# Kernel tuning notes

Hardware: AMD Instinct MI355X
Metric: run time of the kernel (lower is better)

Reference implementation:

```python
import jax, jax.numpy as jnp
import numpy as np

N_HEAD = 16  # head_dim = C // N_HEAD = 128


def setup_inputs() -> dict:
    key = jax.random.key(0)
    k1, k2, k3 = jax.random.split(key, 3)
    B, T, C = 2, 2048, 2048
    x = jax.random.normal(k1, (B, T, C), dtype=jnp.float32)
    # c_attn: Linear(C, 3*C), no bias; stored as (in, out) for x @ W
    w_attn = jax.random.normal(k2, (C, 3 * C), dtype=jnp.float32) * (1.0 / np.sqrt(C))
    # c_proj: Linear(C, C), no bias
    w_proj = jax.random.normal(k3, (C, C), dtype=jnp.float32) * (1.0 / np.sqrt(C))
    return {"x": x, "w_attn": w_attn, "w_proj": w_proj}


def reference(x, w_attn, w_proj):
    B, T, C = x.shape
    H = N_HEAD
    D = C // H  # head dimension
    qkv = x @ w_attn                      # [B, T, 3C]
    q, k, v = jnp.split(qkv, 3, axis=-1)  # each [B, T, C]
    # [B, T, C] -> [B, H, T, D]
    q = q.reshape(B, T, H, D).transpose(0, 2, 1, 3)
    k = k.reshape(B, T, H, D).transpose(0, 2, 1, 3)
    v = v.reshape(B, T, H, D).transpose(0, 2, 1, 3)
    scale = 1.0 / np.sqrt(D).astype(np.float32)
    att = jnp.einsum('bhqd,bhkd->bhqk', q, k) * scale  # [B, H, T, T]
    causal = jnp.tril(jnp.ones((T, T), dtype=bool))
    att = jnp.where(causal[None, None, :, :], att, jnp.float32(-jnp.inf))
    att = jax.nn.softmax(att, axis=-1)
    y = jnp.einsum('bhqk,bhkd->bhqd', att, v)  # [B, H, T, D]
    y = y.transpose(0, 2, 1, 3).reshape(B, T, C)
    # all_reduce is identity with number_of_workers=1; dropout=0 (eval)
    return y @ w_proj
```

## Files before the change

### kernel.cpp

```cpp
#include <hip/hip_runtime.h>
#include <hip/hip_bf16.h>
#include <stdint.h>

#define TLEN 2048
#define CDIM 2048
#define BDIM 2
#define HDIM 16
#define DHEAD 128
#define QROW ((size_t)(2 * CDIM))

typedef __bf16 bf16x8 __attribute__((ext_vector_type(8)));
typedef float f32x4 __attribute__((ext_vector_type(4)));

__device__ __forceinline__ uint16_t f32_to_bf16(float f) {
    uint32_t u = __builtin_bit_cast(uint32_t, f);
    uint32_t r = (u + 0x7FFFu + ((u >> 16) & 1u)) >> 16;
    return (uint16_t)r;
}
__device__ __forceinline__ float bf16_to_f32(uint32_t h) {
    uint32_t u = h << 16;
    return __builtin_bit_cast(float, u);
}

__device__ __forceinline__ void gload_lds16(const uint16_t* g, uint16_t* l) {
    __builtin_amdgcn_global_load_lds(
        (const __attribute__((address_space(1))) uint32_t*)g,
        (__attribute__((address_space(3))) uint32_t*)l, 16, 0, 0);
}

__global__ void cvt_f32_bf16(const float* __restrict__ in, uint16_t* __restrict__ out, int n) {
    int i = (blockIdx.x * blockDim.x + threadIdx.x) * 4;
    if (i + 3 < n) {
        float4 f = *reinterpret_cast<const float4*>(in + i);
        ushort4 o;
        o.x = f32_to_bf16(f.x);
        o.y = f32_to_bf16(f.y);
        o.z = f32_to_bf16(f.z);
        o.w = f32_to_bf16(f.w);
        *reinterpret_cast<ushort4*>(out + i) = o;
    }
}

__global__ __launch_bounds__(256) void transpose_cvt(const float* __restrict__ in,
                                                     uint16_t* __restrict__ out,
                                                     int R, int Cc) {
    __shared__ uint16_t tile[64][65];
    int c0 = blockIdx.x * 64;
    int r0 = blockIdx.y * 64;
    int tc = threadIdx.x & 63;
    int t4 = threadIdx.x >> 6;
    for (int rr = t4; rr < 64; rr += 4) {
        tile[rr][tc] = f32_to_bf16(in[(size_t)(r0 + rr) * Cc + c0 + tc]);
    }
    __syncthreads();
    int wr = threadIdx.x & 63;
    for (int cc = t4; cc < 64; cc += 4) {
        out[(size_t)(c0 + cc) * R + r0 + wr] = tile[wr][cc];
    }
}


#define RD8(P, OFF) (*reinterpret_cast<const bf16x8*>((P) + (OFF)))

#define RDA(DST, P, MB)                                         \
    _Pragma("unroll") for (int mi = 0; mi < 4; mi++) {          \
        DST[mi][0] = RD8(P, rdAo + ((MB) + mi) * 1024 + kblk0); \
        DST[mi][1] = RD8(P, rdAo + ((MB) + mi) * 1024 + kblk1); \
    }

#define RDB4(DST, P)                                        \
    _Pragma("unroll") for (int ni = 0; ni < 4; ni++) {      \
        DST[ni][0] = RD8(P, rdBo + ni * 1024 + kblk0);      \
        DST[ni][1] = RD8(P, rdBo + ni * 1024 + kblk1);      \
    }

#define MFMA32(MB)                                                    \
    _Pragma("unroll") for (int kk = 0; kk < 2; kk++)                  \
    _Pragma("unroll") for (int mi = 0; mi < 4; mi++)                  \
    _Pragma("unroll") for (int ni = 0; ni < 4; ni++)                  \
        acc[(MB) + mi][ni] = __builtin_amdgcn_mfma_f32_16x16x32_bf16( \
            aA[mi][kk], bB[ni][kk], acc[(MB) + mi][ni], 0, 0, 0);

#define TILE(S, T)                                           \
    {                                                        \
        const int k0 = (T) * 64;                             \
        const uint16_t* pA = As + ((S) + wrow) * 8192;       \
        const uint16_t* pB = Bs + ((S) + bsel) * 8192;       \
        RDB4(bB, pB)                                         \
        RDA(aA, pA, 0)                                       \
        asm volatile("s_waitcnt lgkmcnt(8)" ::: "memory");   \
        __builtin_amdgcn_s_barrier();      \
        if ((T) + 2 < nt) {                                  \
            stB((S), 0, k0 + 128);                           \
            stB((S), 1, k0 + 128);                           \
        }                                                    \
        asm volatile("s_waitcnt lgkmcnt(0)" ::: "memory");   \
        __builtin_amdgcn_sched_barrier(0);                   \
        __builtin_amdgcn_s_setprio(1);                       \
        MFMA32(0)                                            \
        __builtin_amdgcn_s_setprio(0);                       \
        RDA(aA, pA, 4)                                       \
        asm volatile("s_waitcnt lgkmcnt(0)" ::: "memory");   \
        __builtin_amdgcn_s_barrier();      \
        if ((T) + 2 < nt) {                                  \
            stA((S), 0, k0 + 128);                           \
            stA((S), 1, k0 + 128);                           \
        }                                                    \
        __builtin_amdgcn_sched_barrier(0);                   \
        __builtin_amdgcn_s_setprio(1);                       \
        MFMA32(4)                                            \
        __builtin_amdgcn_s_setprio(0);                       \
        if ((T) + 2 < nt) {                                  \
            asm volatile("s_waitcnt vmcnt(8)" ::: "memory"); \
        } else if ((T) + 1 < nt) {                           \
            asm volatile("s_waitcnt vmcnt(0)" ::: "memory"); \
        }                                                    \
        __builtin_amdgcn_s_barrier();       \
        __builtin_amdgcn_sched_barrier(0);                   \
    }

template <int MODE>
__global__ __launch_bounds__(512, 2) void gemm_bf16_256(const uint16_t* __restrict__ A,
                                                        const uint16_t* __restrict__ Bt,
                                                        void* __restrict__ Cp,
                                                        uint16_t* __restrict__ vt,
                                                        int M, int N, int K, int xm) {
    __shared__ __align__(16) uint16_t lds[65536];
    uint16_t* const As = lds;
    uint16_t* const Bs = lds + 32768;

    const int tid = threadIdx.x;
    const int wave = tid >> 6;
    const int lane = tid & 63;
    const int l15 = lane & 15;
    const int quad = lane >> 4;
    const int wrow = wave >> 2;
    const int wcol = wave & 3;
    const int bsel = wcol >> 1;

    const int gm = gridDim.y, gn = gridDim.x;
    const int flat = blockIdx.y * gn + blockIdx.x;
    const int xcd = flat & 7;
    const int j = flat >> 3;
    const int xn = 8 / xm;
    const int RM = gm / xm;
    const int RN = gn / xn;
    const int m_blk = (xcd / xn) * RM + (j % RM);
    const int n_blk = (xcd % xn) * RN + (j / RM);
    const int m0 = m_blk * 256;
    const int n0 = n_blk * 256;

    const int srow = wave * 8 + (lane >> 3);
    const int scol = ((lane & 7) ^ (lane >> 3)) * 8;
    const uint16_t* Ag = A + (size_t)(m0 + srow) * K + scol;
    const uint16_t* Bg = Bt + (size_t)(n0 + srow) * K + scol;
    const int ldsoff = wave * 512;

    const int rdAo = l15 * 64;
    const int rdBo = ((wcol & 1) * 64 + l15) * 64;
    const int kblk0 = (quad ^ (l15 & 7)) * 8;
    const int kblk1 = ((4 + quad) ^ (l15 & 7)) * 8;

    const int nt = K >> 6;
    f32x4 acc[8][4] = {};
    bf16x8 aA[4][2], bB[4][2];

    auto stA = [&](int sb, int h, int kk) {
        const uint16_t* s = Ag + (size_t)(h * 128) * K + kk;
        uint16_t* d = As + (sb + h) * 8192 + ldsoff;
        gload_lds16(s, d);
        gload_lds16(s + (size_t)64 * K, d + 4096);
    };
    auto stB = [&](int sb, int h, int kk) {
        const uint16_t* s = Bg + (size_t)(h * 128) * K + kk;
        uint16_t* d = Bs + (sb + h) * 8192 + ldsoff;
        gload_lds16(s, d);
        gload_lds16(s + (size_t)64 * K, d + 4096);
    };

    stB(0, 0, 0);
    stB(0, 1, 0);
    stA(0, 0, 0);
    stA(0, 1, 0);
    stB(2, 0, 64);
    stB(2, 1, 64);
    stA(2, 0, 64);
    stA(2, 1, 64);
    asm volatile("s_waitcnt vmcnt(8)" ::: "memory");
    __builtin_amdgcn_s_barrier();
    __builtin_amdgcn_sched_barrier(0);

    for (int t = 0; t < nt; t += 2) {
        TILE(0, t)
        TILE(2, t + 1)
    }

    const bool vmode = (MODE == 2) && (n0 >= 2 * CDIM);
#pragma unroll
    for (int mi = 0; mi < 8; mi++)
#pragma unroll
        for (int ni = 0; ni < 4; ni++) {
            if (vmode) {
                int col = n0 + wcol * 64 + ni * 16 + l15;
                int vcol = col - 2 * CDIM;
                int hh = vcol >> 7, d = vcol & 127;
                int rowm = m0 + wrow * 128 + mi * 16 + quad * 4;
                int bb = rowm >> 11, tt = rowm & 2047;
                uint32_t lo = (uint32_t)f32_to_bf16(acc[mi][ni][0]) |
                              ((uint32_t)f32_to_bf16(acc[mi][ni][1]) << 16);
                uint32_t hi = (uint32_t)f32_to_bf16(acc[mi][ni][2]) |
                              ((uint32_t)f32_to_bf16(acc[mi][ni][3]) << 16);
                *reinterpret_cast<uint2*>(
                    vt + ((size_t)((bb * HDIM + hh) * DHEAD + d)) * TLEN + tt) =
                    make_uint2(lo, hi);
            } else {
#pragma unroll
                for (int r = 0; r < 4; r++) {
                    int row = m0 + wrow * 128 + mi * 16 + quad * 4 + r;
                    int col = n0 + wcol * 64 + ni * 16 + l15;
                    float v = acc[mi][ni][r];
                    if (MODE == 2)
                        ((uint16_t*)Cp)[(size_t)row * (2 * CDIM) + col] = f32_to_bf16(v);
                    else if (MODE == 1)
                        ((uint16_t*)Cp)[(size_t)row * N + col] = f32_to_bf16(v);
                    else
                        ((float*)Cp)[(size_t)row * N + col] = v;
                }
            }
        }
}

#define ATT_C1 0.12751743f
#define ATT_C2 17.3123405f

__global__ __launch_bounds__(256) void attn_mfma3(const uint16_t* __restrict__ qkv,
                                                  const uint16_t* __restrict__ vtg,
                                                  uint16_t* __restrict__ y) {
    __shared__ __align__(16) uint16_t Ks[64 * 128];
    __shared__ __align__(16) uint16_t Vts[128 * 64];
    __shared__ __align__(16) uint16_t Ps[4][32 * 72];

    const int tid = threadIdx.x;
    const int wave = tid >> 6;
    const int lane = tid & 63;
    const int l15 = lane & 15;
    const int quad = lane >> 4;
    const int h = blockIdx.y;
    const int b = blockIdx.z;
    const int qblk = (int)gridDim.x - 1 - (int)blockIdx.x;
    const int qbase = qblk * 128 + wave * 32;
    const int kmax = qbase + 31;

    const uint16_t* kg = qkv + (size_t)b * TLEN * QROW + CDIM + h * DHEAD;
    const uint16_t* vg = vtg + (size_t)(b * HDIM + h) * DHEAD * TLEN;
    uint16_t* PsW = Ps[wave];

    int koff[4], voff[4];
#pragma unroll
    for (int i = 0; i < 4; i++) {
        int Lb = (wave * 4 + i) * 64 + lane;
        int key = Lb >> 4;
        int ck = (Lb & 15) ^ (key & 15);
        koff[i] = key * (int)QROW + ck * 8;
        int d = Lb >> 3;
        int cv = (Lb & 7) ^ (d & 7);
        voff[i] = d * TLEN + cv * 8;
    }

    bf16x8 qfrag[2][4];
#pragma unroll
    for (int m = 0; m < 2; m++) {
        const uint16_t* qp =
            qkv + (size_t)(b * TLEN + qbase + m * 16 + l15) * QROW + h * DHEAD + quad * 8;
#pragma unroll
        for (int kc = 0; kc < 4; kc++)
            qfrag[m][kc] = *reinterpret_cast<const bf16x8*>(qp + kc * 32);
    }

    f32x4 oacc[2][8] = {};
    float psum[2] = {0.f, 0.f};

    const int diagT = qblk * 2 + (wave >> 1);
    const int ntiles = qblk * 2 + 2;

    for (int t = 0; t < ntiles; t++) {
        const int j0 = t * 64;
        if (t > 0) __syncthreads();
        {
            const uint16_t* kj = kg + (size_t)j0 * QROW;
            const uint16_t* vj = vg + j0;
#pragma unroll
            for (int i = 0; i < 4; i++) {
                gload_lds16(kj + koff[i], Ks + (wave * 4 + i) * 512);
                gload_lds16(vj + voff[i], Vts + (wave * 4 + i) * 512);
            }
        }
        __syncthreads();
        if (t > diagT) continue;

        const bool masked = (t == diagT);
        const int n0max = masked ? ((kmax - j0) >> 4) : 3;

        f32x4 st[4][2];
#pragma unroll
        for (int n0 = 0; n0 < 4; n0++) {
            if (masked && n0 > n0max) continue;
            bf16x8 kf[4];
#pragma unroll
            for (int kc = 0; kc < 4; kc++) {
                int cpr = (kc * 4 + quad) ^ l15;
                kf[kc] = *reinterpret_cast<const bf16x8*>(
                    Ks + (n0 * 16 + l15) * 128 + cpr * 8);
            }
#pragma unroll
            for (int m = 0; m < 2; m++) {
                f32x4 acc = {};
#pragma unroll
                for (int kc = 0; kc < 4; kc++)
                    acc = __builtin_amdgcn_mfma_f32_16x16x32_bf16(
                        kf[kc], qfrag[m][kc], acc, 0, 0, 0);
                st[n0][m] = acc;
            }
        }

#pragma unroll
        for (int n0 = 0; n0 < 4; n0++) {
            if (masked && n0 > n0max) continue;
#pragma unroll
            for (int m = 0; m < 2; m++) {
                uint32_t pk0, pk1;
                float pv[4];
#pragma unroll
                for (int r = 0; r < 4; r++) {
                    float p = exp2f(st[n0][m][r] * ATT_C1 - ATT_C2);
                    if (masked) {
                        int key = j0 + n0 * 16 + quad * 4 + r;
                        int q = qbase + m * 16 + l15;
                        if (key > q) p = 0.f;
                    }
                    uint32_t pb = f32_to_bf16(p);
                    pv[r] = bf16_to_f32(pb);
                    if (r == 0) pk0 = pb;
                    else if (r == 1) pk0 |= pb << 16;
                    else if (r == 2) pk1 = pb;
                    else pk1 |= pb << 16;
                }
                psum[m] += (pv[0] + pv[1]) + (pv[2] + pv[3]);
                *reinterpret_cast<uint2*>(PsW + (m * 16 + l15) * 72 + n0 * 16 + quad * 4) =
                    make_uint2(pk0, pk1);
            }
        }

        const int kcend = masked ? (((kmax - j0) >> 5) + 1) : 2;
#pragma unroll
        for (int kc = 0; kc < 2; kc++) {
            if (kc >= kcend) continue;
            bf16x8 pf[2];
#pragma unroll
            for (int m = 0; m < 2; m++)
                pf[m] = *reinterpret_cast<const bf16x8*>(
                    PsW + (m * 16 + l15) * 72 + kc * 32 + quad * 8);
#pragma unroll
            for (int n0 = 0; n0 < 8; n0++) {
                int cpr = (kc * 4 + quad) ^ (l15 & 7);
                bf16x8 vf = *reinterpret_cast<const bf16x8*>(
                    Vts + (n0 * 16 + l15) * 64 + cpr * 8);
#pragma unroll
                for (int m = 0; m < 2; m++)
                    oacc[m][n0] = __builtin_amdgcn_mfma_f32_16x16x32_bf16(
                        pf[m], vf, oacc[m][n0], 0, 0, 0);
            }
        }
    }

#pragma unroll
    for (int m = 0; m < 2; m++) {
        float s = psum[m];
        s += __shfl_xor(s, 16);
        s += __shfl_xor(s, 32);
        psum[m] = 1.0f / s;
    }
    uint16_t* ybase = y + (size_t)(b * TLEN + qbase) * CDIM + h * DHEAD;
#pragma unroll
    for (int m = 0; m < 2; m++)
#pragma unroll
        for (int r = 0; r < 4; r++) {
            float inv = __shfl(psum[m], quad * 4 + r);
#pragma unroll
            for (int n0 = 0; n0 < 8; n0++)
                ybase[(size_t)(m * 16 + quad * 4 + r) * CDIM + n0 * 16 + l15] =
                    f32_to_bf16(oacc[m][n0][r] * inv);
        }
}

extern "C" void kernel_launch(void* const* d_in, const int* in_sizes, int n_in,
                              void* d_out, int out_size, void* d_ws, size_t ws_size,
                              hipStream_t stream) {
    const float* x = (const float*)d_in[0];
    const float* w_attn = (const float*)d_in[1];
    const float* w_proj = (const float*)d_in[2];
    float* out = (float*)d_out;

    const int M = BDIM * TLEN;
    const int K = CDIM;
    const int N3 = 3 * CDIM;

    char* ws = (char*)d_ws;
    uint16_t* xb = (uint16_t*)(ws);
    uint16_t* waT = (uint16_t*)(ws + 16777216);
    uint16_t* wpT = (uint16_t*)(ws + 41943040);
    uint16_t* qkp = (uint16_t*)(ws + 50331648);
    uint16_t* vtb = (uint16_t*)(ws + 83886080);
    uint16_t* yb = (uint16_t*)(ws + 100663296);

    cvt_f32_bf16<<<(M * K / 4 + 255) / 256, 256, 0, stream>>>(x, xb, M * K);
    transpose_cvt<<<dim3(N3 / 64, K / 64), 256, 0, stream>>>(w_attn, waT, K, N3);
    transpose_cvt<<<dim3(K / 64, K / 64), 256, 0, stream>>>(w_proj, wpT, K, K);
    gemm_bf16_256<2><<<dim3(N3 / 256, M / 256), 512, 0, stream>>>(xb, waT, (void*)qkp, vtb, M, N3, K, 2);
    attn_mfma3<<<dim3(TLEN / 128, HDIM, BDIM), 256, 0, stream>>>(qkp, vtb, yb);
    gemm_bf16_256<0><<<dim3(K / 256, M / 256), 512, 0, stream>>>(yb, wpT, (void*)out, nullptr, M, K, K, 4);
}
```

Before: 428.6 us.

## Prefetch next K/V tile into registers during attention compute

The attention loop now issues global loads for the next K and V tile into registers before computing on the current tile, then stores them to LDS after a barrier. Previously the direct global-to-LDS loads were issued and waited on at the start of each iteration, which exposed their latency. This is a register-staged software pipeline. It costs extra VGPRs, which may lower occupancy, and it adds an extra barrier per iteration.

```diff
diff --git a/kernel.cpp b/kernel.cpp
--- a/kernel.cpp
+++ b/kernel.cpp
@@ -68,10 +68,10 @@
         DST[mi][1] = RD8(P, rdAo + ((MB) + mi) * 1024 + kblk1); \
     }
 
-#define RDB4(DST, P)                                        \
-    _Pragma("unroll") for (int ni = 0; ni < 4; ni++) {      \
-        DST[ni][0] = RD8(P, rdBo + ni * 1024 + kblk0);      \
-        DST[ni][1] = RD8(P, rdBo + ni * 1024 + kblk1);      \
+#define RDB4(DST, P)                                   \
+    _Pragma("unroll") for (int ni = 0; ni < 4; ni++) { \
+        DST[ni][0] = RD8(P, rdBo + ni * 1024 + kblk0); \
+        DST[ni][1] = RD8(P, rdBo + ni * 1024 + kblk1); \
     }
 
 #define MFMA32(MB)                                                    \
@@ -283,94 +283,112 @@
     const int diagT = qblk * 2 + (wave >> 1);
     const int ntiles = qblk * 2 + 2;
 
+#pragma unroll
+    for (int i = 0; i < 4; i++) {
+        gload_lds16(kg + koff[i], Ks + (wave * 4 + i) * 512);
+        gload_lds16(vg + voff[i], Vts + (wave * 4 + i) * 512);
+    }
+    __syncthreads();
+
+    uint4 kpre[4], vpre[4];
     for (int t = 0; t < ntiles; t++) {
-        const int j0 = t * 64;
-        if (t > 0) __syncthreads();
-        {
-            const uint16_t* kj = kg + (size_t)j0 * QROW;
-            const uint16_t* vj = vg + j0;
+        const bool havenext = (t + 1 < ntiles);
+        if (havenext) {
+            const uint16_t* kj = kg + (size_t)(t + 1) * 64 * QROW;
+            const uint16_t* vj = vg + (t + 1) * 64;
 #pragma unroll
             for (int i = 0; i < 4; i++) {
-                gload_lds16(kj + koff[i], Ks + (wave * 4 + i) * 512);
-                gload_lds16(vj + voff[i], Vts + (wave * 4 + i) * 512);
+                kpre[i] = *reinterpret_cast<const uint4*>(kj + koff[i]);
+                vpre[i] = *reinterpret_cast<const uint4*>(vj + voff[i]);
+            }
+        }
+
+        if (t <= diagT) {
+            const int j0 = t * 64;
+            const bool masked = (t == diagT);
+            const int n0max = masked ? ((kmax - j0) >> 4) : 3;
+
+            f32x4 st[4][2];
+#pragma unroll
+            for (int n0 = 0; n0 < 4; n0++) {
+                if (masked && n0 > n0max) continue;
+                bf16x8 kf[4];
+#pragma unroll
+                for (int kc = 0; kc < 4; kc++) {
+                    int cpr = (kc * 4 + quad) ^ l15;
+                    kf[kc] = *reinterpret_cast<const bf16x8*>(
+                        Ks + (n0 * 16 + l15) * 128 + cpr * 8);
+                }
+#pragma unroll
+                for (int m = 0; m < 2; m++) {
+                    f32x4 acc = {};
+#pragma unroll
+                    for (int kc = 0; kc < 4; kc++)
+                        acc = __builtin_amdgcn_mfma_f32_16x16x32_bf16(
+                            kf[kc], qfrag[m][kc], acc, 0, 0, 0);
+                    st[n0][m] = acc;
+                }
+            }
+
+#pragma unroll
+            for (int n0 = 0; n0 < 4; n0++) {
+                if (masked && n0 > n0max) continue;
+#pragma unroll
+                for (int m = 0; m < 2; m++) {
+                    uint32_t pk0, pk1;
+                    float pv[4];
+#pragma unroll
+                    for (int r = 0; r < 4; r++) {
+                        float p = exp2f(st[n0][m][r] * ATT_C1 - ATT_C2);
+                        if (masked) {
+                            int key = j0 + n0 * 16 + quad * 4 + r;
+                            int q = qbase + m * 16 + l15;
+                            if (key > q) p = 0.f;
+                        }
+                        uint32_t pb = f32_to_bf16(p);
+                        pv[r] = bf16_to_f32(pb);
+                        if (r == 0) pk0 = pb;
+                        else if (r == 1) pk0 |= pb << 16;
+                        else if (r == 2) pk1 = pb;
+                        else pk1 |= pb << 16;
+                    }
+                    psum[m] += (pv[0] + pv[1]) + (pv[2] + pv[3]);
+                    *reinterpret_cast<uint2*>(PsW + (m * 16 + l15) * 72 + n0 * 16 + quad * 4) =
+                        make_uint2(pk0, pk1);
+                }
+            }
+
+            const int kcend = masked ? (((kmax - j0) >> 5) + 1) : 2;
+#pragma unroll
+            for (int kc = 0; kc < 2; kc++) {
+                if (kc >= kcend) continue;
+                bf16x8 pf[2];
+#pragma unroll
+                for (int m = 0; m < 2; m++)
+                    pf[m] = *reinterpret_cast<const bf16x8*>(
+                        PsW + (m * 16 + l15) * 72 + kc * 32 + quad * 8);
+#pragma unroll
+                for (int n0 = 0; n0 < 8; n0++) {
+                    int cpr = (kc * 4 + quad) ^ (l15 & 7);
+                    bf16x8 vf = *reinterpret_cast<const bf16x8*>(
+                        Vts + (n0 * 16 + l15) * 64 + cpr * 8);
+#pragma unroll
+                    for (int m = 0; m < 2; m++)
+                        oacc[m][n0] = __builtin_amdgcn_mfma_f32_16x16x32_bf16(
+                            pf[m], vf, oacc[m][n0], 0, 0, 0);
+                }
+            }
+        }
+
+        __syncthreads();
+        if (havenext) {
+#pragma unroll
+            for (int i = 0; i < 4; i++) {
+                *reinterpret_cast<uint4*>(Ks + (wave * 4 + i) * 512 + lane * 8) = kpre[i];
+                *reinterpret_cast<uint4*>(Vts + (wave * 4 + i) * 512 + lane * 8) = vpre[i];
             }
         }
         __syncthreads();
-        if (t > diagT) continue;
-
-        const bool masked = (t == diagT);
-        const int n0max = masked ? ((kmax - j0) >> 4) : 3;
-
-        f32x4 st[4][2];
-#pragma unroll
-        for (int n0 = 0; n0 < 4; n0++) {
-            if (masked && n0 > n0max) continue;
-            bf16x8 kf[4];
-#pragma unroll
-            for (int kc = 0; kc < 4; kc++) {
-                int cpr = (kc * 4 + quad) ^ l15;
-                kf[kc] = *reinterpret_cast<const bf16x8*>(
-                    Ks + (n0 * 16 + l15) * 128 + cpr * 8);
-            }
-#pragma unroll
-            for (int m = 0; m < 2; m++) {
-                f32x4 acc = {};
-#pragma unroll
-                for (int kc = 0; kc < 4; kc++)
-                    acc = __builtin_amdgcn_mfma_f32_16x16x32_bf16(
-                        kf[kc], qfrag[m][kc], acc, 0, 0, 0);
-                st[n0][m] = acc;
-            }
-        }
-
-#pragma unroll
-        for (int n0 = 0; n0 < 4; n0++) {
-            if (masked && n0 > n0max) continue;
-#pragma unroll
-            for (int m = 0; m < 2; m++) {
-                uint32_t pk0, pk1;
-                float pv[4];
-#pragma unroll
-                for (int r = 0; r < 4; r++) {
-                    float p = exp2f(st[n0][m][r] * ATT_C1 - ATT_C2);
-                    if (masked) {
-                        int key = j0 + n0 * 16 + quad * 4 + r;
-                        int q = qbase + m * 16 + l15;
-                        if (key > q) p = 0.f;
-                    }
-                    uint32_t pb = f32_to_bf16(p);
-                    pv[r] = bf16_to_f32(pb);
-                    if (r == 0) pk0 = pb;
-                    else if (r == 1) pk0 |= pb << 16;
-                    else if (r == 2) pk1 = pb;
-                    else pk1 |= pb << 16;
-                }
-                psum[m] += (pv[0] + pv[1]) + (pv[2] + pv[3]);
-                *reinterpret_cast<uint2*>(PsW + (m * 16 + l15) * 72 + n0 * 16 + quad * 4) =
-                    make_uint2(pk0, pk1);
-            }
-        }
-
-        const int kcend = masked ? (((kmax - j0) >> 5) + 1) : 2;
-#pragma unroll
-        for (int kc = 0; kc < 2; kc++) {
-            if (kc >= kcend) continue;
-            bf16x8 pf[2];
-#pragma unroll
-            for (int m = 0; m < 2; m++)
-                pf[m] = *reinterpret_cast<const bf16x8*>(
-                    PsW + (m * 16 + l15) * 72 + kc * 32 + quad * 8);
-#pragma unroll
-            for (int n0 = 0; n0 < 8; n0++) {
-                int cpr = (kc * 4 + quad) ^ (l15 & 7);
-                bf16x8 vf = *reinterpret_cast<const bf16x8*>(
-                    Vts + (n0 * 16 + l15) * 64 + cpr * 8);
-#pragma unroll
-                for (int m = 0; m < 2; m++)
-                    oacc[m][n0] = __builtin_amdgcn_mfma_f32_16x16x32_bf16(
-                        pf[m], vf, oacc[m][n0], 0, 0, 0);
-            }
-        }
     }
 
 #pragma unroll
```

Result: slower. 502.1 us (+17.1%).

## Add 256x128 tiled projection GEMM with XCD-aware block remapping

Applied to the files above, without the earlier changes.

Replaces the 256x256-tile output projection GEMM with a dedicated 256x128-tile kernel, doubling the block count so all compute units get work. Blocks are remapped so neighbouring tiles land on the same XCD for L2 reuse, and the LDS pipeline is restructured with separately staged A halves and B tiles. Smaller tiles lower per-block arithmetic intensity and raise total global loads of A.

```diff
diff --git a/kernel.cpp b/kernel.cpp
--- a/kernel.cpp
+++ b/kernel.cpp
@@ -68,10 +68,10 @@
         DST[mi][1] = RD8(P, rdAo + ((MB) + mi) * 1024 + kblk1); \
     }
 
-#define RDB4(DST, P)                                        \
-    _Pragma("unroll") for (int ni = 0; ni < 4; ni++) {      \
-        DST[ni][0] = RD8(P, rdBo + ni * 1024 + kblk0);      \
-        DST[ni][1] = RD8(P, rdBo + ni * 1024 + kblk1);      \
+#define RDB4(DST, P)                                   \
+    _Pragma("unroll") for (int ni = 0; ni < 4; ni++) { \
+        DST[ni][0] = RD8(P, rdBo + ni * 1024 + kblk0); \
+        DST[ni][1] = RD8(P, rdBo + ni * 1024 + kblk1); \
     }
 
 #define MFMA32(MB)                                                    \
@@ -230,6 +230,117 @@
         }
 }
 
+__global__ __launch_bounds__(512, 2) void gemm_proj_256x128(
+    const uint16_t* __restrict__ A, const uint16_t* __restrict__ Bt,
+    float* __restrict__ C, int M, int N, int K) {
+    __shared__ __align__(16) uint16_t lds[49152];
+    uint16_t* const As = lds;
+    uint16_t* const Bs = lds + 32768;
+
+    const int tid = threadIdx.x;
+    const int wave = tid >> 6;
+    const int lane = tid & 63;
+    const int l15 = lane & 15;
+    const int quad = lane >> 4;
+    const int wrow = wave >> 1;
+    const int wcol = wave & 1;
+    const int aunit = wrow >> 1;
+
+    const int gn = gridDim.x;
+    const int flat = blockIdx.y * gn + blockIdx.x;
+    const int xcd = flat & 7;
+    const int j = flat >> 3;
+    const int m_blk = (xcd >> 1) * 4 + (j & 3);
+    const int n_blk = (xcd & 1) * 8 + (j >> 2);
+    const int m0 = m_blk * 256;
+    const int n0 = n_blk * 128;
+
+    const int srow = wave * 8 + (lane >> 3);
+    const int scol = ((lane & 7) ^ (lane >> 3)) * 8;
+    const uint16_t* Ag = A + (size_t)(m0 + srow) * K + scol;
+    const uint16_t* Bg = Bt + (size_t)(n0 + srow) * K + scol;
+    const int ldsoff = wave * 512;
+
+    const int rdAo = ((wrow & 1) * 64 + l15) * 64;
+    const int rdBo = (wcol * 64 + l15) * 64;
+    const int kblk0 = (quad ^ (l15 & 7)) * 8;
+    const int kblk1 = ((4 + quad) ^ (l15 & 7)) * 8;
+
+    const int nt = K >> 6;
+    f32x4 acc[4][4] = {};
+    bf16x8 aA[4][2], bB[4][2];
+
+    auto stA = [&](int sb, int h, int kk) {
+        const uint16_t* s = Ag + (size_t)(h * 128) * K + kk;
+        uint16_t* d = As + (sb + h) * 8192 + ldsoff;
+        gload_lds16(s, d);
+        gload_lds16(s + (size_t)64 * K, d + 4096);
+    };
+    auto stB = [&](int sb, int kk) {
+        const uint16_t* s = Bg + kk;
+        uint16_t* d = Bs + sb * 8192 + ldsoff;
+        gload_lds16(s, d);
+        gload_lds16(s + (size_t)64 * K, d + 4096);
+    };
+
+    stB(0, 0);
+    stA(0, 0, 0);
+    stA(0, 1, 0);
+    stB(1, 64);
+    stA(2, 0, 64);
+    stA(2, 1, 64);
+    asm volatile("s_waitcnt vmcnt(6)" ::: "memory");
+    __builtin_amdgcn_s_barrier();
+    __builtin_amdgcn_sched_barrier(0);
+
+#define PTILE(SA, SB, T)                                     \
+    {                                                        \
+        const int k0 = (T) * 64;                             \
+        const uint16_t* pA = As + ((SA) + aunit) * 8192;     \
+        const uint16_t* pB = Bs + (SB) * 8192;               \
+        RDB4(bB, pB)                                         \
+        RDA(aA, pA, 0)                                       \
+        asm volatile("s_waitcnt lgkmcnt(8)" ::: "memory");   \
+        __builtin_amdgcn_s_barrier();      \
+        if ((T) + 2 < nt) stB((SB), k0 + 128);               \
+        asm volatile("s_waitcnt lgkmcnt(0)" ::: "memory");   \
+        __builtin_amdgcn_sched_barrier(0);                   \
+        __builtin_amdgcn_s_setprio(1);                       \
+        MFMA32(0)                                            \
+        __builtin_amdgcn_s_setprio(0);                       \
+        __builtin_amdgcn_s_barrier();      \
+        if ((T) + 2 < nt) {                                  \
+            stA((SA), 0, k0 + 128);                          \
+            stA((SA), 1, k0 + 128);                          \
+        }                                                    \
+        __builtin_amdgcn_sched_barrier(0);                   \
+        if ((T) + 2 < nt) {                                  \
+            asm volatile("s_waitcnt vmcnt(6)" ::: "memory"); \
+        } else if ((T) + 1 < nt) {                           \
+            asm volatile("s_waitcnt vmcnt(0)" ::: "memory"); \
+        }                                                    \
+        __builtin_amdgcn_s_barrier();       \
+        __builtin_amdgcn_sched_barrier(0);                   \
+    }
+
+    for (int t = 0; t < nt; t += 2) {
+        PTILE(0, 0, t)
+        PTILE(2, 1, t + 1)
+    }
+#undef PTILE
+
+#pragma unroll
+    for (int mi = 0; mi < 4; mi++)
+#pragma unroll
+        for (int ni = 0; ni < 4; ni++)
+#pragma unroll
+            for (int r = 0; r < 4; r++) {
+                int row = m0 + wrow * 64 + mi * 16 + quad * 4 + r;
+                int col = n0 + wcol * 64 + ni * 16 + l15;
+                C[(size_t)row * N + col] = acc[mi][ni][r];
+            }
+}
+
 #define ATT_C1 0.12751743f
 #define ATT_C2 17.3123405f
 
@@ -418,5 +529,5 @@
     transpose_cvt<<<dim3(K / 64, K / 64), 256, 0, stream>>>(w_proj, wpT, K, K);
     gemm_bf16_256<2><<<dim3(N3 / 256, M / 256), 512, 0, stream>>>(xb, waT, (void*)qkp, vtb, M, N3, K, 2);
     attn_mfma3<<<dim3(TLEN / 128, HDIM, BDIM), 256, 0, stream>>>(qkp, vtb, yb);
-    gemm_bf16_256<0><<<dim3(K / 256, M / 256), 512, 0, stream>>>(yb, wpT, (void*)out, nullptr, M, K, K, 4);
-}
+    gemm_proj_256x128<<<dim3(K / 128, M / 256), 512, 0, stream>>>(yb, wpT, out, M, K, K);
+}
```

New measurement: 414.1 us. -3.4%, faster.
